# Kernel tuning notes

Hardware: AMD Instinct MI355X
Metric: run time of the kernel (lower is better)

## Reference

```python
import jax, jax.numpy as jnp
import numpy as np
from jax import lax

D_MODEL = 512
D_STATE = 16
D_CONV = 4
DT_RANK = 32  # ceil(512/16)
BATCH = 4
SEQ = 2048
FN = 32


def setup_inputs() -> dict:
    key = jax.random.key(0)
    ks = jax.random.split(key, 12)
    s = 0.02
    d, n, r = D_MODEL, D_STATE, DT_RANK
    return {
        "atoms": jax.random.normal(ks[0], (BATCH, SEQ, d), jnp.float32),
        # normalized "adjacency"-like matrix so delta_p = dis_dense @ delta stays O(1)
        "dis_dense": jax.random.uniform(ks[1], (BATCH, SEQ, SEQ), jnp.float32) / SEQ,
        "gpt_emb": jax.random.normal(ks[2], (BATCH, d), jnp.float32),
        "fg_emb": jax.random.normal(ks[3], (BATCH, FN, d), jnp.float32),
        "in_proj_w": jax.random.normal(ks[4], (2 * d, d), jnp.float32) * s,
        "conv_w": jax.random.normal(ks[5], (d, 1, D_CONV), jnp.float32) * s,  # depthwise OIW
        "conv_b": jnp.zeros((d,), jnp.float32),
        "x_proj_w": jax.random.normal(ks[6], (r + 2 * n, d), jnp.float32) * s,
        "dt_proj_w": jax.random.normal(ks[7], (d, r), jnp.float32) * s,
        "dt_proj_b": jnp.full((d,), 0.5, jnp.float32),
        "A_log": jnp.log(jnp.broadcast_to(jnp.arange(1, n + 1, dtype=jnp.float32), (d, n))),
        "D_param": jnp.ones((d,), jnp.float32),
        "out_proj_w": jax.random.normal(ks[8], (d, d), jnp.float32) * s,
        "film_w1": jax.random.normal(ks[9], (d, d), jnp.float32) * s,
        "film_b1": jnp.zeros((d,), jnp.float32),
        "film_w2": jax.random.normal(ks[10], (2 * d, d), jnp.float32) * s,
        "film_b2": jnp.zeros((2 * d,), jnp.float32),
    }


def reference(atoms, dis_dense, gpt_emb, fg_emb,
              in_proj_w, conv_w, conv_b, x_proj_w, dt_proj_w, dt_proj_b,
              A_log, D_param, out_proj_w, film_w1, film_b1, film_w2, film_b2):
    b, l, d = atoms.shape
    n = A_log.shape[1]

    # --- CrossAttentionFusion: Q=atoms, K/V=fg_emb ---
    scores = jnp.einsum('bld,bfd->blf', atoms, fg_emb) / (d ** 0.5)
    attn = jax.nn.softmax(scores, axis=-1)
    x = atoms + jnp.einsum('blf,bfd->bld', attn, fg_emb)

    # --- FiLM modulation from gpt_emb ---
    h = jax.nn.silu(gpt_emb @ film_w1.T + film_b1)
    gamma, beta = jnp.split(h @ film_w2.T + film_b2, 2, axis=-1)
    x = x * gamma[:, None, :] + beta[:, None, :]

    # --- in_proj and split into (x, res) ---
    xs, res = jnp.split(x @ in_proj_w.T, 2, axis=-1)

    # --- depthwise causal-padded conv1d, truncate to l ---
    xc = jnp.transpose(xs, (0, 2, 1))  # [b, d, l]
    xc = lax.conv_general_dilated(xc, conv_w, window_strides=(1,),
                                  padding=[(D_CONV - 1, D_CONV - 1)],
                                  feature_group_count=d)[:, :, :l]
    xc = xc + conv_b[None, :, None]
    u = jax.nn.silu(jnp.transpose(xc, (0, 2, 1)))  # [b, l, d]

    # --- SSM ---
    A = -jnp.exp(A_log)                      # [d, n]
    x_dbl = u @ x_proj_w.T                   # [b, l, r+2n]
    delta, Bm, Cm = jnp.split(x_dbl, [DT_RANK, DT_RANK + n], axis=-1)
    delta = jax.nn.softplus(delta @ dt_proj_w.T + dt_proj_b)  # [b, l, d]
    delta_p = jnp.einsum('blk,bkd->bld', dis_dense, delta)     # graph-mixed delta

    deltaA = jnp.exp(delta_p[..., None] * A)                   # [b, l, d, n]
    deltaB_u = delta_p[..., None] * Bm[:, :, None, :] * u[..., None]  # [b, l, d, n]

    def step(carry, inp):
        dA_t, dBu_t, C_t = inp
        carry = dA_t * carry + dBu_t                # [b, d, n]
        y_t = jnp.einsum('bdn,bn->bd', carry, C_t)
        return carry, y_t

    init = jnp.zeros((b, d, n), deltaA.dtype)
    _, ys = lax.scan(step, init,
                     (jnp.moveaxis(deltaA, 1, 0),
                      jnp.moveaxis(deltaB_u, 1, 0),
                      jnp.moveaxis(Cm, 1, 0)))
    y = jnp.moveaxis(ys, 0, 1) + u * D_param       # [b, l, d]

    # --- gate, out_proj, nonfinite -> 0 ---
    y = y * jax.nn.silu(res)
    out = y @ out_proj_w.T
    return jnp.where(jnp.isfinite(out), out, 0.0)
```

## Files before the change

kernel.cpp:

```cpp
#include <hip/hip_runtime.h>
#include <stdint.h>

#define D_MODEL 512
#define D_STATE 16
#define DT_RANK 32
#define SEQ 2048
#define NBATCH 4
#define FN 32
#define CHUNK 16
#define NCHUNK 128
#define DPPLANE ((size_t)8192*D_MODEL)

typedef unsigned short u16;
using s16x8 = __attribute__((ext_vector_type(8))) short;
using f32x4 = __attribute__((ext_vector_type(4))) float;
using f32x8 = __attribute__((ext_vector_type(8))) float;
using bf16x8 = __attribute__((ext_vector_type(8))) __bf16;

typedef __attribute__((address_space(3))) void lds_void;
typedef __attribute__((address_space(1))) const void glb_void;

__device__ __forceinline__ void gload16(const void* g, void* l) {
  __builtin_amdgcn_global_load_lds((glb_void*)g, (lds_void*)l, 16, 0, 0);
}

__device__ inline u16 f2bf(float f) {
  uint32_t u = __float_as_uint(f);
  u += 0x7FFFu + ((u >> 16) & 1u);
  return (u16)(u >> 16);
}
__device__ __forceinline__ float bf2f(u16 v) {
  return __uint_as_float((uint32_t)v << 16);
}

__device__ __forceinline__ s16x8 pack8bf(float4 lo, float4 hi) {
  f32x8 v;
  v[0] = lo.x; v[1] = lo.y; v[2] = lo.z; v[3] = lo.w;
  v[4] = hi.x; v[5] = hi.y; v[6] = hi.z; v[7] = hi.w;
  bf16x8 b = __builtin_convertvector(v, bf16x8);
  return __builtin_bit_cast(s16x8, b);
}
__device__ __forceinline__ ushort4 pack4bf(float a, float b, float c, float d) {
  ushort4 o; o.x = f2bf(a); o.y = f2bf(b); o.z = f2bf(c); o.w = f2bf(d);
  return o;
}

__global__ __launch_bounds__(256) void film1_kernel(
    const float* __restrict__ gpt, const float* __restrict__ w1,
    const float* __restrict__ b1, float* __restrict__ h)
{
  int b = blockIdx.y, r0 = blockIdx.x*16, t = threadIdx.x;
  __shared__ float g[D_MODEL];
  for (int i = t; i < D_MODEL; i += 256) g[i] = gpt[b*D_MODEL + i];
  __syncthreads();
  int r = r0 + (t >> 4), ln = t & 15;
  const float* wr = &w1[(size_t)r*D_MODEL + ln*32];
  const float* gg = &g[ln*32];
  float s = 0.f;
  #pragma unroll
  for (int k = 0; k < 32; k += 4) {
    float4 w = *(const float4*)&wr[k];
    s += w.x*gg[k] + w.y*gg[k+1] + w.z*gg[k+2] + w.w*gg[k+3];
  }
  s += __shfl_down(s, 8); s += __shfl_down(s, 4);
  s += __shfl_down(s, 2); s += __shfl_down(s, 1);
  if (ln == 0) { float v = s + b1[r]; h[b*D_MODEL + r] = v / (1.f + expf(-v)); }
}

__global__ __launch_bounds__(256) void film2_kernel(
    const float* __restrict__ h, const float* __restrict__ w2,
    const float* __restrict__ b2, float* __restrict__ gb)
{
  int b = blockIdx.y, r0 = blockIdx.x*16, t = threadIdx.x;
  __shared__ float hs[D_MODEL];
  for (int i = t; i < D_MODEL; i += 256) hs[i] = h[b*D_MODEL + i];
  __syncthreads();
  int r = r0 + (t >> 4), ln = t & 15;
  const float* wr = &w2[(size_t)r*D_MODEL + ln*32];
  const float* gg = &hs[ln*32];
  float s = 0.f;
  #pragma unroll
  for (int k = 0; k < 32; k += 4) {
    float4 w = *(const float4*)&wr[k];
    s += w.x*gg[k] + w.y*gg[k+1] + w.z*gg[k+2] + w.w*gg[k+3];
  }
  s += __shfl_down(s, 8); s += __shfl_down(s, 4);
  s += __shfl_down(s, 2); s += __shfl_down(s, 1);
  if (ln == 0) gb[b*1024 + r] = s + b2[r];
}

__global__ __launch_bounds__(256) void prep_kernel(
    const float* __restrict__ fg, const float* __restrict__ inw,
    const float* __restrict__ outw, const float* __restrict__ dtw,
    const float* __restrict__ xpw,
    u16* __restrict__ fgpad, u16* __restrict__ inwbf,
    u16* __restrict__ outwbf, u16* __restrict__ wcomb)
{
  int blk = blockIdx.x, t = threadIdx.x;
  if (blk < 512) {
    int row = blk & 127, b = blk >> 7;
    u16* dst = &fgpad[((size_t)b*128 + row)*D_MODEL];
    if (row < FN) {
      const float* src = &fg[((size_t)b*FN + row)*D_MODEL];
      float2 v = *(const float2*)&src[t*2];
      dst[t*2] = f2bf(v.x); dst[t*2+1] = f2bf(v.y);
    } else {
      dst[t*2] = 0; dst[t*2+1] = 0;
    }
  } else if (blk < 1536) {
    int row = blk - 512;
    float2 v = *(const float2*)&inw[(size_t)row*D_MODEL + t*2];
    inwbf[(size_t)row*D_MODEL + t*2]     = f2bf(v.x);
    inwbf[(size_t)row*D_MODEL + t*2 + 1] = f2bf(v.y);
  } else if (blk < 2048) {
    int row = blk - 1536;
    float2 v = *(const float2*)&outw[(size_t)row*D_MODEL + t*2];
    outwbf[(size_t)row*D_MODEL + t*2]     = f2bf(v.x);
    outwbf[(size_t)row*D_MODEL + t*2 + 1] = f2bf(v.y);
  } else {
    int row = blk - 2048;
    if (row < D_MODEL) {
      __shared__ float dr[DT_RANK];
      if (t < DT_RANK) dr[t] = dtw[row*DT_RANK + t];
      __syncthreads();
      for (int k = t; k < D_MODEL; k += 256) {
        float s = 0.f;
        #pragma unroll
        for (int r = 0; r < DT_RANK; r++) s += dr[r] * xpw[r*D_MODEL + k];
        wcomb[(size_t)row*D_MODEL + k] = f2bf(s);
      }
    } else if (row < D_MODEL + 32) {
      for (int k = t; k < D_MODEL; k += 256)
        wcomb[(size_t)row*D_MODEL + k] = f2bf(xpw[(size_t)(DT_RANK + row - D_MODEL)*D_MODEL + k]);
    } else {
      for (int k = t; k < D_MODEL; k += 256)
        wcomb[(size_t)row*D_MODEL + k] = 0;
    }
  }
}

__global__ __launch_bounds__(256) void pv_film_kernel(
    const float* __restrict__ atoms, const float* __restrict__ fg,
    const float* __restrict__ scores, const float* __restrict__ gb,
    u16* __restrict__ xout)
{
  int wave = threadIdx.x >> 6, lane = threadIdx.x & 63;
  int row = blockIdx.x*4 + wave;
  int b = row >> 11;
  float s = scores[(size_t)row*128 + (lane & 31)] * 0.04419417382415922f;
  float m = s;
  #pragma unroll
  for (int o = 16; o; o >>= 1) m = fmaxf(m, __shfl_xor(m, o));
  float e = __expf(s - m);
  float sum = e;
  #pragma unroll
  for (int o = 16; o; o >>= 1) sum += __shfl_xor(sum, o);
  float my_attn = e / sum;

  int d0 = lane*8;
  const float* arow = &atoms[(size_t)row*D_MODEL + d0];
  float4 acc0 = *(const float4*)&arow[0];
  float4 acc1 = *(const float4*)&arow[4];
  const float* fgb = &fg[(size_t)b*FN*D_MODEL + d0];
  #pragma unroll 8
  for (int f = 0; f < FN; f++) {
    float w = __shfl(my_attn, f);
    float4 g0 = *(const float4*)&fgb[(size_t)f*D_MODEL];
    float4 g1 = *(const float4*)&fgb[(size_t)f*D_MODEL + 4];
    acc0.x += w*g0.x; acc0.y += w*g0.y; acc0.z += w*g0.z; acc0.w += w*g0.w;
    acc1.x += w*g1.x; acc1.y += w*g1.y; acc1.z += w*g1.z; acc1.w += w*g1.w;
  }
  const float* gbg = &gb[(size_t)b*1024 + d0];
  float4 gm0 = *(const float4*)&gbg[0];
  float4 gm1 = *(const float4*)&gbg[4];
  float4 bt0 = *(const float4*)&gbg[D_MODEL];
  float4 bt1 = *(const float4*)&gbg[D_MODEL + 4];
  s16x8 o;
  o[0] = (short)f2bf(acc0.x*gm0.x + bt0.x);
  o[1] = (short)f2bf(acc0.y*gm0.y + bt0.y);
  o[2] = (short)f2bf(acc0.z*gm0.z + bt0.z);
  o[3] = (short)f2bf(acc0.w*gm0.w + bt0.w);
  o[4] = (short)f2bf(acc1.x*gm1.x + bt1.x);
  o[5] = (short)f2bf(acc1.y*gm1.y + bt1.y);
  o[6] = (short)f2bf(acc1.z*gm1.z + bt1.z);
  o[7] = (short)f2bf(acc1.w*gm1.w + bt1.w);
  *(s16x8*)&xout[(size_t)row*D_MODEL + d0] = o;
}

__global__ __launch_bounds__(256) void cvt_bf16_kernel(
    const float* __restrict__ in, u16* __restrict__ out, int n4)
{
  int i = blockIdx.x*256 + threadIdx.x;
  if (i >= n4) return;
  float4 v = *(const float4*)&in[(size_t)i*4];
  ushort4 o; o.x = f2bf(v.x); o.y = f2bf(v.y); o.z = f2bf(v.z); o.w = f2bf(v.w);
  *(ushort4*)&out[(size_t)i*4] = o;
}

__global__ __launch_bounds__(256) void gemm_bt64_kernel(
    const u16* __restrict__ A, const u16* __restrict__ B, void* __restrict__ Cv_,
    int M, int N, int K, int outMode)
{
  int gx = gridDim.x, gy = gridDim.y;
  int flat = blockIdx.x + gx*blockIdx.y;
  int cpx = (gx*gy) >> 3;
  flat = (flat & 7)*cpx + (flat >> 3);
  int bx = flat % gx, by = flat / gx;
  int m0 = by * 64, n0 = bx * 128;
  __shared__ u16 As[2][64][32];
  __shared__ u16 Bs[2][128][32];
  int tid = threadIdx.x, lane = tid & 63, wave = tid >> 6;
  int wm = (wave >> 1) * 32, wn = (wave & 1) * 64;
  int fr = lane & 15, fk = (lane >> 4) * 8;
  int srow = tid >> 2, scol = (tid & 3) * 8;
  const u16* abase  = &A[(size_t)(m0 + srow)*K + scol];
  const u16* b0base = &B[(size_t)(n0 + srow)*K + scol];
  const u16* b1base = &B[(size_t)(n0 + 64 + srow)*K + scol];
  gload16(abase,  &As[0][srow][scol]);
  gload16(b0base, &Bs[0][srow][scol]);
  gload16(b1base, &Bs[0][64 + srow][scol]);
  __syncthreads();
  f32x4 acc[2][4] = {};
  int NT = K >> 5, cur = 0;
  for (int t = 0; t < NT; t++) {
    int nxt = cur ^ 1;
    if (t + 1 < NT) {
      int k0 = (t + 1) << 5;
      gload16(&abase[k0],  &As[nxt][srow][scol]);
      gload16(&b0base[k0], &Bs[nxt][srow][scol]);
      gload16(&b1base[k0], &Bs[nxt][64 + srow][scol]);
    }
    s16x8 af[2], bf[4];
    #pragma unroll
    for (int i = 0; i < 2; i++) af[i] = *(const s16x8*)(&As[cur][wm + i*16 + fr][fk]);
    #pragma unroll
    for (int i = 0; i < 4; i++) bf[i] = *(const s16x8*)(&Bs[cur][wn + i*16 + fr][fk]);
    #pragma unroll
    for (int mi = 0; mi < 2; mi++)
      #pragma unroll
      for (int ni = 0; ni < 4; ni++)
        acc[mi][ni] = __builtin_amdgcn_mfma_f32_16x16x32_bf16(af[mi], bf[ni], acc[mi][ni], 0, 0, 0);
    __syncthreads();
    cur = nxt;
  }
  int cr = (lane >> 4) * 4, cc = lane & 15;
  if (outMode == 2) {
    u16* C = (u16*)Cv_;
    #pragma unroll
    for (int mi = 0; mi < 2; mi++)
      #pragma unroll
      for (int ni = 0; ni < 4; ni++) {
        int rowb = m0 + wm + mi*16 + cr, col = n0 + wn + ni*16 + cc;
        #pragma unroll
        for (int r = 0; r < 4; r++)
          C[(size_t)(rowb + r)*N + col] = f2bf(acc[mi][ni][r]);
      }
  } else {
    float* C = (float*)Cv_;
    #pragma unroll
    for (int mi = 0; mi < 2; mi++)
      #pragma unroll
      for (int ni = 0; ni < 4; ni++) {
        int rowb = m0 + wm + mi*16 + cr, col = n0 + wn + ni*16 + cc;
        #pragma unroll
        for (int r = 0; r < 4; r++) {
          float v = acc[mi][ni][r];
          if (outMode == 1 && !isfinite(v)) v = 0.f;
          C[(size_t)(rowb + r)*N + col] = v;
        }
      }
  }
}

__global__ __launch_bounds__(256) void gemm_f32a_kernel(
    const float* __restrict__ Ag, const u16* __restrict__ Bg, float* __restrict__ Cg,
    int M, int N, int K, long long azs, long long bzs, long long czs,
    int clampFinite, int swz)
{
  int gx = gridDim.x, gy = gridDim.y;
  int flat = blockIdx.x + gx*(blockIdx.y + gy*blockIdx.z);
  if (swz) {
    int cpx = (gx*gy*(int)gridDim.z) >> 3;
    flat = (flat & 7)*cpx + (flat >> 3);
  }
  int bx = flat % gx, tmp = flat / gx;
  int by = tmp % gy, bz = tmp / gy;
  const float* A = Ag + (size_t)bz * azs;
  const u16* B = Bg + (size_t)bz * bzs;
  float* C = Cg + (size_t)bz * czs;
  int m0 = by * 128, n0 = bx * 128;
  __shared__ u16 As[128][32];
  __shared__ u16 Bs[128][32];
  int tid = threadIdx.x, lane = tid & 63, wave = tid >> 6;
  int wm = (wave >> 1) * 64, wn = (wave & 1) * 64;
  int fr = lane & 15, fk = (lane >> 4) * 8;
  int srow = tid >> 2, scol = (tid & 3) * 8;
  f32x4 acc[4][4] = {};
  for (int k0 = 0; k0 < K; k0 += 32) {
    const float* a0p = &A[(size_t)(m0 + srow)*K + k0 + scol];
    const float* a1p = &A[(size_t)(m0 + 64 + srow)*K + k0 + scol];
    float4 a00 = *(const float4*)&a0p[0];
    float4 a01 = *(const float4*)&a0p[4];
    float4 a10 = *(const float4*)&a1p[0];
    float4 a11 = *(const float4*)&a1p[4];
    gload16(&B[(size_t)(n0 + srow)*K + k0 + scol],      &Bs[srow][scol]);
    gload16(&B[(size_t)(n0 + 64 + srow)*K + k0 + scol], &Bs[64 + srow][scol]);
    *(s16x8*)&As[srow][scol]      = pack8bf(a00, a01);
    *(s16x8*)&As[64 + srow][scol] = pack8bf(a10, a11);
    __syncthreads();
    s16x8 af[4], bf[4];
    #pragma unroll
    for (int i = 0; i < 4; i++) af[i] = *(const s16x8*)(&As[wm + i*16 + fr][fk]);
    #pragma unroll
    for (int i = 0; i < 4; i++) bf[i] = *(const s16x8*)(&Bs[wn + i*16 + fr][fk]);
    #pragma unroll
    for (int mi = 0; mi < 4; mi++)
      #pragma unroll
      for (int ni = 0; ni < 4; ni++)
        acc[mi][ni] = __builtin_amdgcn_mfma_f32_16x16x32_bf16(af[mi], bf[ni], acc[mi][ni], 0, 0, 0);
    __syncthreads();
  }
  int cr = (lane >> 4) * 4, cc = lane & 15;
  #pragma unroll
  for (int mi = 0; mi < 4; mi++)
    #pragma unroll
    for (int ni = 0; ni < 4; ni++) {
      int rowb = m0 + wm + mi*16 + cr, col = n0 + wn + ni*16 + cc;
      #pragma unroll
      for (int r = 0; r < 4; r++) {
        float v = acc[mi][ni][r];
        if (clampFinite && !isfinite(v)) v = 0.f;
        C[(size_t)(rowb + r)*N + col] = v;
      }
    }
}

__global__ __launch_bounds__(256) void gemm_dpbf_splitk_kernel(
    const u16* __restrict__ disbf, const u16* __restrict__ deltaT,
    u16* __restrict__ dpp)
{
  int gx = gridDim.x, gy = gridDim.y;
  int flat = blockIdx.x + gx*(blockIdx.y + gy*blockIdx.z);
  int cpx = (gx*gy*(int)gridDim.z) >> 3;
  flat = (flat & 7)*cpx + (flat >> 3);
  int bx = flat % gx, tmp = flat / gx;
  int by = tmp % gy, bz = tmp / gy;
  int b = bz >> 2, ks = bz & 3;
  const u16* A = disbf  + (size_t)b*SEQ*SEQ     + ks*512;
  const u16* B = deltaT + (size_t)b*D_MODEL*SEQ + ks*512;
  u16*       C = dpp    + (size_t)ks*DPPLANE    + (size_t)b*SEQ*D_MODEL;
  int m0 = by * 128, n0 = bx * 128;
  __shared__ u16 As[128][32];
  __shared__ u16 Bs[128][32];
  int tid = threadIdx.x, lane = tid & 63, wave = tid >> 6;
  int wm = (wave >> 1) * 64, wn = (wave & 1) * 64;
  int fr = lane & 15, fk = (lane >> 4) * 8;
  int srow = tid >> 2, scol = (tid & 3) * 8;
  f32x4 acc[4][4] = {};
  for (int k0 = 0; k0 < 512; k0 += 32) {
    gload16(&A[(size_t)(m0 + srow)*SEQ + k0 + scol],      &As[srow][scol]);
    gload16(&A[(size_t)(m0 + 64 + srow)*SEQ + k0 + scol], &As[64 + srow][scol]);
    gload16(&B[(size_t)(n0 + srow)*SEQ + k0 + scol],      &Bs[srow][scol]);
    gload16(&B[(size_t)(n0 + 64 + srow)*SEQ + k0 + scol], &Bs[64 + srow][scol]);
    __syncthreads();
    s16x8 af[4], bf[4];
    #pragma unroll
    for (int i = 0; i < 4; i++) af[i] = *(const s16x8*)(&As[wm + i*16 + fr][fk]);
    #pragma unroll
    for (int i = 0; i < 4; i++) bf[i] = *(const s16x8*)(&Bs[wn + i*16 + fr][fk]);
    #pragma unroll
    for (int mi = 0; mi < 4; mi++)
      #pragma unroll
      for (int ni = 0; ni < 4; ni++)
        acc[mi][ni] = __builtin_amdgcn_mfma_f32_16x16x32_bf16(af[mi], bf[ni], acc[mi][ni], 0, 0, 0);
    __syncthreads();
  }
  int cr = (lane >> 4) * 4, cc = lane & 15;
  #pragma unroll
  for (int mi = 0; mi < 4; mi++)
    #pragma unroll
    for (int ni = 0; ni < 4; ni++) {
      int rowb = m0 + wm + mi*16 + cr, col = n0 + wn + ni*16 + cc;
      #pragma unroll
      for (int r = 0; r < 4; r++)
        C[(size_t)(rowb + r)*D_MODEL + col] = f2bf(acc[mi][ni][r]);
    }
}

__global__ __launch_bounds__(256) void gemm_delta_kernel(
    const u16* __restrict__ A, const u16* __restrict__ B,
    const float* __restrict__ dtb, u16* __restrict__ deltaT,
    float* __restrict__ Bv, float* __restrict__ Cv)
{
  int gx = gridDim.x, gy = gridDim.y;
  int flat = blockIdx.x + gx*blockIdx.y;
  int cpx = (gx*gy) >> 3;
  flat = (flat & 7)*cpx + (flat >> 3);
  int bx = flat % gx, by = flat / gx;
  int m0 = by * 64, n0 = bx * 128;
  __shared__ u16 As[64][32];
  __shared__ u16 Bs[128][32];
  int tid = threadIdx.x, lane = tid & 63, wave = tid >> 6;
  int wm = (wave >> 1) * 32, wn = (wave & 1) * 64;
  int fr = lane & 15, fk = (lane >> 4) * 8;
  int srow = tid >> 2, scol = (tid & 3) * 8;
  f32x4 acc[2][4] = {};
  for (int k0 = 0; k0 < D_MODEL; k0 += 32) {
    gload16(&A[(size_t)(m0 + srow)*D_MODEL + k0 + scol],      &As[srow][scol]);
    gload16(&B[(size_t)(n0 + srow)*D_MODEL + k0 + scol],      &Bs[srow][scol]);
    gload16(&B[(size_t)(n0 + 64 + srow)*D_MODEL + k0 + scol], &Bs[64 + srow][scol]);
    __syncthreads();
    s16x8 af[2], bf[4];
    #pragma unroll
    for (int i = 0; i < 2; i++) af[i] = *(const s16x8*)(&As[wm + i*16 + fr][fk]);
    #pragma unroll
    for (int i = 0; i < 4; i++) bf[i] = *(const s16x8*)(&Bs[wn + i*16 + fr][fk]);
    #pragma unroll
    for (int mi = 0; mi < 2; mi++)
      #pragma unroll
      for (int ni = 0; ni < 4; ni++)
        acc[mi][ni] = __builtin_amdgcn_mfma_f32_16x16x32_bf16(af[mi], bf[ni], acc[mi][ni], 0, 0, 0);
    __syncthreads();
  }
  int cr = (lane >> 4) * 4, cc = lane & 15;
  #pragma unroll
  for (int mi = 0; mi < 2; mi++)
    #pragma unroll
    for (int ni = 0; ni < 4; ni++) {
      int rowb = m0 + wm + mi*16 + cr, col = n0 + wn + ni*16 + cc;
      if (col < D_MODEL) {
        float bias = dtb[col];
        #pragma unroll
        for (int r = 0; r < 4; r++) {
          float v = acc[mi][ni][r] + bias;
          v = (v > 20.f) ? v : log1pf(expf(v));
          int gr = rowb + r;
          deltaT[((size_t)(gr >> 11)*D_MODEL + col)*SEQ + (gr & (SEQ-1))] = f2bf(v);
        }
      } else if (col < D_MODEL + 16) {
        #pragma unroll
        for (int r = 0; r < 4; r++)
          Bv[(size_t)(rowb + r)*D_STATE + (col - D_MODEL)] = acc[mi][ni][r];
      } else if (col < D_MODEL + 32) {
        #pragma unroll
        for (int r = 0; r < 4; r++)
          Cv[(size_t)(rowb + r)*D_STATE + (col - D_MODEL - 16)] = acc[mi][ni][r];
      }
    }
}

__global__ __launch_bounds__(256) void conv_silu_kernel(
    const u16* __restrict__ xsres, const float* __restrict__ cw,
    const float* __restrict__ cb, u16* __restrict__ ubf)
{
  int idx = blockIdx.x*256 + threadIdx.x;
  int d = (idx & 127) * 4;
  int row = idx >> 7;
  int l = row & (SEQ - 1);
  float w[4][4];
  #pragma unroll
  for (int c = 0; c < 4; c++) *(float4*)w[c] = *(const float4*)&cw[(d + c)*4];
  float4 acc = *(const float4*)&cb[d];
  #pragma unroll
  for (int k = 0; k < 4; k++) {
    int li = l - 3 + k;
    if (li >= 0) {
      ushort4 v = *(const ushort4*)&xsres[(size_t)(row - 3 + k)*1024 + d];
      acc.x += bf2f(v.x)*w[0][k]; acc.y += bf2f(v.y)*w[1][k];
      acc.z += bf2f(v.z)*w[2][k]; acc.w += bf2f(v.w)*w[3][k];
    }
  }
  float4 o;
  o.x = acc.x/(1.f+expf(-acc.x)); o.y = acc.y/(1.f+expf(-acc.y));
  o.z = acc.z/(1.f+expf(-acc.z)); o.w = acc.w/(1.f+expf(-acc.w));
  ushort4 ob;
  ob.x = f2bf(o.x); ob.y = f2bf(o.y); ob.z = f2bf(o.z); ob.w = f2bf(o.w);
  *(ushort4*)&ubf[(size_t)row*D_MODEL + d] = ob;
}

__global__ __launch_bounds__(256) void scanA_kernel(
    const u16* __restrict__ dpp, const u16* __restrict__ ubf,
    const float* __restrict__ Bv, const float* __restrict__ A_log,
    u16* __restrict__ dpf, u16* __restrict__ slocal, float* __restrict__ sumdp_out)
{
  int d = blockIdx.x*256 + threadIdx.x;
  int c = blockIdx.y, b = blockIdx.z;
  __shared__ float Bs[CHUNK][D_STATE];
  int t = threadIdx.x;
  size_t lbase = (size_t)b*SEQ + c*CHUNK;
  Bs[t >> 4][t & 15] = Bv[(lbase + (t >> 4))*D_STATE + (t & 15)];
  float a[D_STATE];
  #pragma unroll
  for (int n = 0; n < D_STATE; n += 4) {
    float4 v = *(const float4*)&A_log[(size_t)d*D_STATE + n];
    a[n] = -expf(v.x); a[n+1] = -expf(v.y); a[n+2] = -expf(v.z); a[n+3] = -expf(v.w);
  }
  __syncthreads();
  float s[D_STATE];
  #pragma unroll
  for (int n = 0; n < D_STATE; n++) s[n] = 0.f;
  float sd = 0.f;
  for (int j = 0; j < CHUNK; j++) {
    size_t r = lbase + j;
    size_t idx = r*D_MODEL + d;
    float dpv = bf2f(dpp[idx]) + bf2f(dpp[idx + DPPLANE])
              + bf2f(dpp[idx + 2*DPPLANE]) + bf2f(dpp[idx + 3*DPPLANE]);
    dpf[idx] = f2bf(dpv);
    float uv  = bf2f(ubf[idx]);
    sd += dpv;
    float dbu = dpv * uv;
    #pragma unroll
    for (int n = 0; n < D_STATE; n++)
      s[n] = __expf(a[n]*dpv)*s[n] + dbu*Bs[j][n];
  }
  size_t obase = ((size_t)b*NCHUNK + c)*D_MODEL + d;
  #pragma unroll
  for (int n = 0; n < D_STATE; n += 4)
    *(ushort4*)&slocal[obase*D_STATE + n] = pack4bf(s[n], s[n+1], s[n+2], s[n+3]);
  sumdp_out[obase] = sd;
}

__global__ __launch_bounds__(256) void scanB_kernel(
    const u16* __restrict__ slocal, const float* __restrict__ sumdp,
    const float* __restrict__ A_log, u16* __restrict__ sIn)
{
  int g = blockIdx.x*256 + threadIdx.x;
  int n = g & 15, d = (g >> 4) & (D_MODEL - 1), b = g >> 13;
  float a = -expf(A_log[d*D_STATE + n]);
  float s = 0.f;
  for (int c = 0; c < NCHUNK; c++) {
    size_t idx = ((size_t)b*NCHUNK + c)*D_MODEL + d;
    sIn[idx*D_STATE + n] = f2bf(s);
    s = __expf(a * sumdp[idx]) * s + bf2f(slocal[idx*D_STATE + n]);
  }
}

__global__ __launch_bounds__(256) void scanC_kernel(
    const u16* __restrict__ dp, const u16* __restrict__ ubf,
    const float* __restrict__ Bv, const float* __restrict__ Cv,
    const float* __restrict__ A_log, const float* __restrict__ Dp,
    const u16* __restrict__ xsres, const u16* __restrict__ sIn,
    u16* __restrict__ yout)
{
  int d = blockIdx.x*256 + threadIdx.x;
  int c = blockIdx.y, b = blockIdx.z;
  __shared__ float Bs[CHUNK][D_STATE];
  __shared__ float Cs[CHUNK][D_STATE];
  int t = threadIdx.x;
  size_t lbase = (size_t)b*SEQ + c*CHUNK;
  Bs[t >> 4][t & 15] = Bv[(lbase + (t >> 4))*D_STATE + (t & 15)];
  Cs[t >> 4][t & 15] = Cv[(lbase + (t >> 4))*D_STATE + (t & 15)];
  float a[D_STATE];
  #pragma unroll
  for (int n = 0; n < D_STATE; n += 4) {
    float4 v = *(const float4*)&A_log[(size_t)d*D_STATE + n];
    a[n] = -expf(v.x); a[n+1] = -expf(v.y); a[n+2] = -expf(v.z); a[n+3] = -expf(v.w);
  }
  float s[D_STATE];
  size_t ibase = (((size_t)b*NCHUNK + c)*D_MODEL + d)*D_STATE;
  #pragma unroll
  for (int n = 0; n < D_STATE; n += 4) {
    ushort4 v = *(const ushort4*)&sIn[ibase + n];
    s[n] = bf2f(v.x); s[n+1] = bf2f(v.y); s[n+2] = bf2f(v.z); s[n+3] = bf2f(v.w);
  }
  float dparam = Dp[d];
  __syncthreads();
  for (int j = 0; j < CHUNK; j++) {
    size_t r = lbase + j;
    float dpv = bf2f(dp[r*D_MODEL + d]);
    float uv  = bf2f(ubf[r*D_MODEL + d]);
    float dbu = dpv * uv;
    float y = 0.f;
    #pragma unroll
    for (int n = 0; n < D_STATE; n++) {
      s[n] = __expf(a[n]*dpv)*s[n] + dbu*Bs[j][n];
      y += s[n]*Cs[j][n];
    }
    y += uv * dparam;
    float rr = bf2f(xsres[r*1024 + D_MODEL + d]);
    y *= rr/(1.f + __expf(-rr));
    yout[r*D_MODEL + d] = f2bf(y);
  }
}

extern "C" void kernel_launch(void* const* d_in, const int* in_sizes, int n_in,
                              void* d_out, int out_size, void* d_ws, size_t ws_size,
                              hipStream_t stream)
{
  const float* atoms  = (const float*)d_in[0];
  const float* dis    = (const float*)d_in[1];
  const float* gpt    = (const float*)d_in[2];
  const float* fg     = (const float*)d_in[3];
  const float* inw    = (const float*)d_in[4];
  const float* convw  = (const float*)d_in[5];
  const float* convb  = (const float*)d_in[6];
  const float* xpw    = (const float*)d_in[7];
  const float* dtw    = (const float*)d_in[8];
  const float* dtb    = (const float*)d_in[9];
  const float* A_log  = (const float*)d_in[10];
  const float* Dparam = (const float*)d_in[11];
  const float* outw   = (const float*)d_in[12];
  const float* fw1    = (const float*)d_in[13];
  const float* fb1    = (const float*)d_in[14];
  const float* fw2    = (const float*)d_in[15];
  const float* fb2    = (const float*)d_in[16];

  char* ws = (char*)d_ws;
  size_t off = 0;
  auto alloc = [&](size_t bytes) { char* p = ws + off; off += (bytes + 255) & ~255ull; return p; };
  float* gb     = (float*)alloc((size_t)NBATCH*1024*4);
  float* hbuf   = (float*)alloc((size_t)NBATCH*512*4);
  u16*   fgpad  = (u16*)  alloc((size_t)NBATCH*128*512*2);
  float* scores = (float*)alloc((size_t)NBATCH*2048*128*4);
  u16*   xbf    = (u16*)  alloc((size_t)8192*512*2);
  u16*   inwbf  = (u16*)  alloc((size_t)1024*512*2);
  u16*   outwbf = (u16*)  alloc((size_t)512*512*2);
  u16*   wcomb  = (u16*)  alloc((size_t)640*512*2);
  u16*   xsres  = (u16*)  alloc((size_t)8192*1024*2);
  u16*   dpp    = (u16*)  alloc(4*DPPLANE*2);
  u16*   dpf    = (u16*)  alloc(DPPLANE*2);
  u16*   ubf    = (u16*)  alloc((size_t)8192*512*2);
  float* Bv     = (float*)alloc((size_t)8192*16*4);
  float* Cv     = (float*)alloc((size_t)8192*16*4);
  u16*   deltaT = (u16*)  alloc((size_t)NBATCH*512*2048*2);
  u16*   slocal = (u16*)  alloc((size_t)NBATCH*NCHUNK*512*16*2);
  float* sumdp  = (float*)alloc((size_t)NBATCH*NCHUNK*512*4);
  u16*   sIn    = (u16*)  alloc((size_t)NBATCH*NCHUNK*512*16*2);
  u16*   disbf  = (u16*)slocal;

  film1_kernel<<<dim3(32, NBATCH), 256, 0, stream>>>(gpt, fw1, fb1, hbuf);
  film2_kernel<<<dim3(64, NBATCH), 256, 0, stream>>>(hbuf, fw2, fb2, gb);
  prep_kernel<<<2688, 256, 0, stream>>>(fg, inw, outw, dtw, xpw, fgpad, inwbf, outwbf, wcomb);
  cvt_bf16_kernel<<<(NBATCH*2048*2048/4)/256, 256, 0, stream>>>(dis, disbf, NBATCH*2048*2048/4);

  gemm_f32a_kernel<<<dim3(1, 2048/128, NBATCH), 256, 0, stream>>>(
      atoms, fgpad, scores, 2048, 128, 512,
      (long long)2048*512, (long long)128*512, (long long)2048*128, 0, 1);
  pv_film_kernel<<<8192/4, 256, 0, stream>>>(atoms, fg, scores, gb, xbf);

  gemm_bt64_kernel<<<dim3(1024/128, 8192/64), 256, 0, stream>>>(
      xbf, inwbf, xsres, 8192, 1024, 512, 2);
  conv_silu_kernel<<<8192*128/256, 256, 0, stream>>>(xsres, convw, convb, ubf);

  gemm_delta_kernel<<<dim3(640/128, 8192/64), 256, 0, stream>>>(
      ubf, wcomb, dtb, deltaT, Bv, Cv);

  gemm_dpbf_splitk_kernel<<<dim3(512/128, 2048/128, NBATCH*4), 256, 0, stream>>>(
      disbf, deltaT, dpp);

  scanA_kernel<<<dim3(2, NCHUNK, NBATCH), 256, 0, stream>>>(dpp, ubf, Bv, A_log, dpf, slocal, sumdp);
  scanB_kernel<<<32768/256, 256, 0, stream>>>(slocal, sumdp, A_log, sIn);
  u16* ybf = xbf;
  scanC_kernel<<<dim3(2, NCHUNK, NBATCH), 256, 0, stream>>>(dpf, ubf, Bv, Cv, A_log, Dparam, xsres, sIn, ybf);

  gemm_bt64_kernel<<<dim3(512/128, 8192/64), 256, 0, stream>>>(
      ybf, outwbf, (float*)d_out, 8192, 512, 512, 1);
}
```

Before: 235.3 us.

## Fuse dis conversion into prep kernel, shrink scores GEMM tile, reuse conv window

The standalone fp32-to-bf16 conversion of the dense distance matrix is folded into prep_kernel as extra blocks, which removes one kernel launch. The scores GEMM moves to 64-row tiles, doubling its block count from 64 to 128 so more CUs are busy. The depthwise conv+SiLU kernel now has each thread produce four consecutive rows from a 7-row window, so neighbouring input rows are reused instead of reloaded. In exchange, the conv kernel uses more registers per thread and launches a quarter as many threads.

```diff
diff --git a/kernel.cpp b/kernel.cpp
--- a/kernel.cpp
+++ b/kernel.cpp
@@ -92,12 +92,18 @@
 __global__ __launch_bounds__(256) void prep_kernel(
     const float* __restrict__ fg, const float* __restrict__ inw,
     const float* __restrict__ outw, const float* __restrict__ dtw,
-    const float* __restrict__ xpw,
+    const float* __restrict__ xpw, const float* __restrict__ dis,
     u16* __restrict__ fgpad, u16* __restrict__ inwbf,
-    u16* __restrict__ outwbf, u16* __restrict__ wcomb)
+    u16* __restrict__ outwbf, u16* __restrict__ wcomb,
+    u16* __restrict__ disbf)
 {
   int blk = blockIdx.x, t = threadIdx.x;
-  if (blk < 512) {
+  if (blk >= 2688) {
+    size_t i = (size_t)(blk - 2688)*256 + t;
+    float4 v = *(const float4*)&dis[i*4];
+    ushort4 o; o.x = f2bf(v.x); o.y = f2bf(v.y); o.z = f2bf(v.z); o.w = f2bf(v.w);
+    *(ushort4*)&disbf[i*4] = o;
+  } else if (blk < 512) {
     int row = blk & 127, b = blk >> 7;
     u16* dst = &fgpad[((size_t)b*128 + row)*D_MODEL];
     if (row < FN) {
@@ -187,16 +193,6 @@
   *(s16x8*)&xout[(size_t)row*D_MODEL + d0] = o;
 }
 
-__global__ __launch_bounds__(256) void cvt_bf16_kernel(
-    const float* __restrict__ in, u16* __restrict__ out, int n4)
-{
-  int i = blockIdx.x*256 + threadIdx.x;
-  if (i >= n4) return;
-  float4 v = *(const float4*)&in[(size_t)i*4];
-  ushort4 o; o.x = f2bf(v.x); o.y = f2bf(v.y); o.z = f2bf(v.z); o.w = f2bf(v.w);
-  *(ushort4*)&out[(size_t)i*4] = o;
-}
-
 __global__ __launch_bounds__(256) void gemm_bt64_kernel(
     const u16* __restrict__ A, const u16* __restrict__ B, void* __restrict__ Cv_,
     int M, int N, int K, int outMode)
@@ -272,49 +268,42 @@
   }
 }
 
-__global__ __launch_bounds__(256) void gemm_f32a_kernel(
+__global__ __launch_bounds__(256) void gemm_f32a64_kernel(
     const float* __restrict__ Ag, const u16* __restrict__ Bg, float* __restrict__ Cg,
-    int M, int N, int K, long long azs, long long bzs, long long czs,
-    int clampFinite, int swz)
+    int M, int N, int K, long long azs, long long bzs, long long czs)
 {
   int gx = gridDim.x, gy = gridDim.y;
   int flat = blockIdx.x + gx*(blockIdx.y + gy*blockIdx.z);
-  if (swz) {
-    int cpx = (gx*gy*(int)gridDim.z) >> 3;
-    flat = (flat & 7)*cpx + (flat >> 3);
-  }
+  int cpx = (gx*gy*(int)gridDim.z) >> 3;
+  flat = (flat & 7)*cpx + (flat >> 3);
   int bx = flat % gx, tmp = flat / gx;
   int by = tmp % gy, bz = tmp / gy;
   const float* A = Ag + (size_t)bz * azs;
   const u16* B = Bg + (size_t)bz * bzs;
   float* C = Cg + (size_t)bz * czs;
-  int m0 = by * 128, n0 = bx * 128;
-  __shared__ u16 As[128][32];
+  int m0 = by * 64, n0 = bx * 128;
+  __shared__ u16 As[64][32];
   __shared__ u16 Bs[128][32];
   int tid = threadIdx.x, lane = tid & 63, wave = tid >> 6;
-  int wm = (wave >> 1) * 64, wn = (wave & 1) * 64;
+  int wm = (wave >> 1) * 32, wn = (wave & 1) * 64;
   int fr = lane & 15, fk = (lane >> 4) * 8;
   int srow = tid >> 2, scol = (tid & 3) * 8;
-  f32x4 acc[4][4] = {};
+  f32x4 acc[2][4] = {};
   for (int k0 = 0; k0 < K; k0 += 32) {
-    const float* a0p = &A[(size_t)(m0 + srow)*K + k0 + scol];
-    const float* a1p = &A[(size_t)(m0 + 64 + srow)*K + k0 + scol];
-    float4 a00 = *(const float4*)&a0p[0];
-    float4 a01 = *(const float4*)&a0p[4];
-    float4 a10 = *(const float4*)&a1p[0];
-    float4 a11 = *(const float4*)&a1p[4];
+    const float* ap = &A[(size_t)(m0 + srow)*K + k0 + scol];
+    float4 a0 = *(const float4*)&ap[0];
+    float4 a1 = *(const float4*)&ap[4];
     gload16(&B[(size_t)(n0 + srow)*K + k0 + scol],      &Bs[srow][scol]);
     gload16(&B[(size_t)(n0 + 64 + srow)*K + k0 + scol], &Bs[64 + srow][scol]);
-    *(s16x8*)&As[srow][scol]      = pack8bf(a00, a01);
-    *(s16x8*)&As[64 + srow][scol] = pack8bf(a10, a11);
+    *(s16x8*)&As[srow][scol] = pack8bf(a0, a1);
     __syncthreads();
-    s16x8 af[4], bf[4];
-    #pragma unroll
-    for (int i = 0; i < 4; i++) af[i] = *(const s16x8*)(&As[wm + i*16 + fr][fk]);
+    s16x8 af[2], bf[4];
+    #pragma unroll
+    for (int i = 0; i < 2; i++) af[i] = *(const s16x8*)(&As[wm + i*16 + fr][fk]);
     #pragma unroll
     for (int i = 0; i < 4; i++) bf[i] = *(const s16x8*)(&Bs[wn + i*16 + fr][fk]);
     #pragma unroll
-    for (int mi = 0; mi < 4; mi++)
+    for (int mi = 0; mi < 2; mi++)
       #pragma unroll
       for (int ni = 0; ni < 4; ni++)
         acc[mi][ni] = __builtin_amdgcn_mfma_f32_16x16x32_bf16(af[mi], bf[ni], acc[mi][ni], 0, 0, 0);
@@ -322,16 +311,13 @@
   }
   int cr = (lane >> 4) * 4, cc = lane & 15;
   #pragma unroll
-  for (int mi = 0; mi < 4; mi++)
+  for (int mi = 0; mi < 2; mi++)
     #pragma unroll
     for (int ni = 0; ni < 4; ni++) {
       int rowb = m0 + wm + mi*16 + cr, col = n0 + wn + ni*16 + cc;
       #pragma unroll
-      for (int r = 0; r < 4; r++) {
-        float v = acc[mi][ni][r];
-        if (clampFinite && !isfinite(v)) v = 0.f;
-        C[(size_t)(rowb + r)*N + col] = v;
-      }
+      for (int r = 0; r < 4; r++)
+        C[(size_t)(rowb + r)*N + col] = acc[mi][ni][r];
     }
 }
 
@@ -454,28 +440,41 @@
     const float* __restrict__ cb, u16* __restrict__ ubf)
 {
   int idx = blockIdx.x*256 + threadIdx.x;
-  int d = (idx & 127) * 4;
-  int row = idx >> 7;
-  int l = row & (SEQ - 1);
+  int dq = idx & 127;
+  int rg = idx >> 7;
+  int d = dq*4;
+  size_t row0 = (size_t)rg*4;
+  int l0 = (int)(row0 & (SEQ - 1));
   float w[4][4];
   #pragma unroll
   for (int c = 0; c < 4; c++) *(float4*)w[c] = *(const float4*)&cw[(d + c)*4];
-  float4 acc = *(const float4*)&cb[d];
-  #pragma unroll
-  for (int k = 0; k < 4; k++) {
-    int li = l - 3 + k;
+  float4 bias = *(const float4*)&cb[d];
+  float4 x[7];
+  #pragma unroll
+  for (int k = 0; k < 7; k++) {
+    int li = l0 - 3 + k;
     if (li >= 0) {
-      ushort4 v = *(const ushort4*)&xsres[(size_t)(row - 3 + k)*1024 + d];
-      acc.x += bf2f(v.x)*w[0][k]; acc.y += bf2f(v.y)*w[1][k];
-      acc.z += bf2f(v.z)*w[2][k]; acc.w += bf2f(v.w)*w[3][k];
-    }
-  }
-  float4 o;
-  o.x = acc.x/(1.f+expf(-acc.x)); o.y = acc.y/(1.f+expf(-acc.y));
-  o.z = acc.z/(1.f+expf(-acc.z)); o.w = acc.w/(1.f+expf(-acc.w));
-  ushort4 ob;
-  ob.x = f2bf(o.x); ob.y = f2bf(o.y); ob.z = f2bf(o.z); ob.w = f2bf(o.w);
-  *(ushort4*)&ubf[(size_t)row*D_MODEL + d] = ob;
+      ushort4 v = *(const ushort4*)&xsres[(row0 - 3 + k)*1024 + d];
+      x[k] = make_float4(bf2f(v.x), bf2f(v.y), bf2f(v.z), bf2f(v.w));
+    } else {
+      x[k] = make_float4(0.f, 0.f, 0.f, 0.f);
+    }
+  }
+  #pragma unroll
+  for (int j = 0; j < 4; j++) {
+    float4 acc = bias;
+    #pragma unroll
+    for (int k = 0; k < 4; k++) {
+      float4 v = x[j + k];
+      acc.x += v.x*w[0][k]; acc.y += v.y*w[1][k];
+      acc.z += v.z*w[2][k]; acc.w += v.w*w[3][k];
+    }
+    float4 o;
+    o.x = acc.x/(1.f+expf(-acc.x)); o.y = acc.y/(1.f+expf(-acc.y));
+    o.z = acc.z/(1.f+expf(-acc.z)); o.w = acc.w/(1.f+expf(-acc.w));
+    ushort4 ob; ob.x = f2bf(o.x); ob.y = f2bf(o.y); ob.z = f2bf(o.z); ob.w = f2bf(o.w);
+    *(ushort4*)&ubf[(row0 + j)*D_MODEL + d] = ob;
+  }
 }
 
 __global__ __launch_bounds__(256) void scanA_kernel(
@@ -630,17 +629,17 @@
 
   film1_kernel<<<dim3(32, NBATCH), 256, 0, stream>>>(gpt, fw1, fb1, hbuf);
   film2_kernel<<<dim3(64, NBATCH), 256, 0, stream>>>(hbuf, fw2, fb2, gb);
-  prep_kernel<<<2688, 256, 0, stream>>>(fg, inw, outw, dtw, xpw, fgpad, inwbf, outwbf, wcomb);
-  cvt_bf16_kernel<<<(NBATCH*2048*2048/4)/256, 256, 0, stream>>>(dis, disbf, NBATCH*2048*2048/4);
-
-  gemm_f32a_kernel<<<dim3(1, 2048/128, NBATCH), 256, 0, stream>>>(
+  prep_kernel<<<2688 + 16384, 256, 0, stream>>>(fg, inw, outw, dtw, xpw, dis,
+                                                fgpad, inwbf, outwbf, wcomb, disbf);
+
+  gemm_f32a64_kernel<<<dim3(1, 2048/64, NBATCH), 256, 0, stream>>>(
       atoms, fgpad, scores, 2048, 128, 512,
-      (long long)2048*512, (long long)128*512, (long long)2048*128, 0, 1);
+      (long long)2048*512, (long long)128*512, (long long)2048*128);
   pv_film_kernel<<<8192/4, 256, 0, stream>>>(atoms, fg, scores, gb, xbf);
 
   gemm_bt64_kernel<<<dim3(1024/128, 8192/64), 256, 0, stream>>>(
       xbf, inwbf, xsres, 8192, 1024, 512, 2);
-  conv_silu_kernel<<<8192*128/256, 256, 0, stream>>>(xsres, convw, convb, ubf);
+  conv_silu_kernel<<<262144/256, 256, 0, stream>>>(xsres, convw, convb, ubf);
 
   gemm_delta_kernel<<<dim3(640/128, 8192/64), 256, 0, stream>>>(
       ubf, wcomb, dtb, deltaT, Bv, Cv);
```

Result: faster. 220.0 us (-6.5%).
